# Optimization experiments

Measured on AMD Instinct MI355X. Metric: run time of the kernel, lower is better.

Reference implementation:

```python
import jax, jax.numpy as jnp
import numpy as np
from itertools import product


def _build_apot_levels(num_bits=8, n=2):
    k = num_bits // n
    groups = []
    for i in range(n):
        vals = [0.0]
        for j in range(2 ** k - 1):
            vals.append(2 ** (-(i + j * n)))
        groups.append(vals)
    levels = set()
    for combo in product(*groups):
        levels.add(round(sum(combo), 14))
    levels = sorted(levels)
    max_v = max(levels) if levels else 1.0
    if max_v > 0:
        levels = [v / max_v for v in levels]
    return levels


def _make_levels(num_bits=8, signed=True):
    levels = _build_apot_levels(num_bits=num_bits, n=2)
    if signed:
        neg = [-v for v in levels[1:]][::-1]
        levels = neg + levels
    return np.asarray(levels, dtype=np.float32)


def setup_inputs() -> dict:
    key = jax.random.key(0)
    x = jax.random.normal(key, (32, 4096, 1024), dtype=jnp.float32)
    alpha = jnp.ones((1,), dtype=jnp.float32)          # learned scalar scale
    levels = jnp.asarray(_make_levels(8, True))         # sorted APoT levels buffer, shape [L]
    return {"x": x, "alpha": alpha, "levels": levels}


def reference(x, alpha, levels):
    a = jnp.abs(alpha) + 1e-8                 # [1], broadcasts
    x_norm = jnp.clip(x / a, -1.0, 1.0)       # signed=True clamp
    x_det = jax.lax.stop_gradient(x_norm)
    L = levels.shape[0]
    # torch.bucketize(right=False) == searchsorted side='left'
    idx_right = jnp.clip(jnp.searchsorted(levels, x_det, side="left"), 0, L - 1)
    idx_left = jnp.clip(idx_right - 1, 0, L - 1)
    right = levels[idx_right]
    left = levels[idx_left]
    choose_right = jnp.abs(x_det - left) > jnp.abs(right - x_det)
    snapped = jnp.where(choose_right, right, left)
    # straight-through estimator
    snapped_ste = x_norm + jax.lax.stop_gradient(snapped - x_norm)
    return a * snapped_ste
```

## Files before the change

kernel.cpp:

```cpp
#include <hip/hip_runtime.h>
#include <float.h>


#define TREE_H 9
#define NNODES (1 << TREE_H)

typedef float floatx4 __attribute__((ext_vector_type(4)));

__device__ __forceinline__ float apot_one(float xi, float a,
                                          const float* __restrict__ eyt,
                                          float lev0, float levmax) {
    float xn = xi / a;
    xn = fminf(fmaxf(xn, -1.0f), 1.0f);
    int idx = 1;
    float lft = lev0;
    float rgt = levmax;
    #pragma unroll
    for (int s = 0; s < TREE_H; ++s) {
        float e = eyt[idx];
        bool go_r = e < xn;
        lft = go_r ? e : lft;
        rgt = go_r ? rgt : e;
        idx = 2 * idx + (go_r ? 1 : 0);
    }
    float d_l = fabsf(xn - lft);
    float d_r = fabsf(rgt - xn);
    return a * ((d_l > d_r) ? rgt : lft);
}

__global__ __launch_bounds__(256) void apot_kernel(
    const float* __restrict__ x,
    const float* __restrict__ alpha,
    const float* __restrict__ levels,
    float* __restrict__ out,
    long long n, long long n4, int L)
{
    __shared__ float eyt[NNODES];
    for (int i = threadIdx.x + 1; i < NNODES; i += blockDim.x) {
        int d = 31 - __clz(i);
        int pos = i - (1 << d);
        int srt = pos * (1 << (TREE_H - d)) + (1 << (TREE_H - 1 - d)) - 1;
        eyt[i] = (srt < L) ? levels[srt] : FLT_MAX;
    }
    __syncthreads();

    float a = fabsf(alpha[0]) + 1e-8f;
    float lev0 = levels[0];
    float levmax = levels[L - 1];

    long long tid = (long long)blockIdx.x * blockDim.x + threadIdx.x;
    long long stride = (long long)gridDim.x * blockDim.x;

    const floatx4* __restrict__ x4 = (const floatx4*)x;
    floatx4* __restrict__ o4 = (floatx4*)out;
    for (long long t = tid; t < n4; t += stride) {
        floatx4 v = x4[t];
        floatx4 ov;
        ov.x = apot_one(v.x, a, eyt, lev0, levmax);
        ov.y = apot_one(v.y, a, eyt, lev0, levmax);
        ov.z = apot_one(v.z, a, eyt, lev0, levmax);
        ov.w = apot_one(v.w, a, eyt, lev0, levmax);
        __builtin_nontemporal_store(ov, &o4[t]);
    }
    for (long long t = n4 * 4 + tid; t < n; t += stride) {
        out[t] = apot_one(x[t], a, eyt, lev0, levmax);
    }
}

extern "C" void kernel_launch(void* const* d_in, const int* in_sizes, int n_in,
                              void* d_out, int out_size, void* d_ws, size_t ws_size,
                              hipStream_t stream) {
    const float* x      = (const float*)d_in[0];
    const float* alpha  = (const float*)d_in[1];
    const float* levels = (const float*)d_in[2];
    float* out = (float*)d_out;

    long long n  = (long long)out_size;
    long long n4 = n >> 2;
    int L = in_sizes[2];

    const int block = 256;
    long long want = (n4 + block - 1) / block;
    if (want < 1) want = 1;
    int grid = (int)(want < 8192 ? want : 8192);

    apot_kernel<<<grid, block, 0, stream>>>(x, alpha, levels, out, n, n4, L);
}
```

Measured before the change: 886.0 us.

## Fold symmetric APoT levels into magnitude search with register-held top tree levels

For L==511 the kernel relies on the level table being symmetric around zero. It searches only the positive half using |x|, with a one-ulp bias so ties on negative inputs resolve the same way as the reference, which shortens the Eytzinger search from 9 to 8 levels. The top three tree levels are kept in registers, leaving only 5 shared-memory lookups per element. A specialised path skips the divide and multiply when alpha==1. This assumes symmetric levels, which the general 511-level input may not satisfy, and it adds code size and register pressure.

```diff
diff --git a/kernel.cpp b/kernel.cpp
--- a/kernel.cpp
+++ b/kernel.cpp
@@ -2,10 +2,106 @@
 #include <float.h>
 
 
+typedef float floatx4 __attribute__((ext_vector_type(4)));
+
+
+template<bool AONE>
+__device__ __forceinline__ float apot_fold(
+    float xi, float a, const float* __restrict__ eyt, float zl,
+    float e1, float e2, float e3, float e4, float e5, float e6, float e7)
+{
+    float xn = AONE ? xi : (xi / a);
+    xn = fminf(fmaxf(xn, -1.0f), 1.0f);
+    bool neg = xn < 0.0f;
+    float u  = fabsf(xn);
+    float us = __uint_as_float(__float_as_uint(u) + (neg ? 1u : 0u));
+
+    float lft = zl;
+    float rgt = FLT_MAX;
+
+    bool g0 = e1 < us;  lft = g0 ? e1 : lft;  rgt = g0 ? rgt : e1;
+    float ea = g0 ? e3 : e2;
+    bool g1 = ea < us;  lft = g1 ? ea : lft;  rgt = g1 ? rgt : ea;
+    float t0 = g1 ? e5 : e4;
+    float t1 = g1 ? e7 : e6;
+    float eb = g0 ? t1 : t0;
+    bool g2 = eb < us;  lft = g2 ? eb : lft;  rgt = g2 ? rgt : eb;
+
+    int idx = 8 + (g0 ? 4 : 0) + (g1 ? 2 : 0) + (g2 ? 1 : 0);
+    #pragma unroll
+    for (int s = 0; s < 5; ++s) {
+        float e = eyt[idx];
+        bool g = e < us;
+        lft = g ? e : lft;
+        rgt = g ? rgt : e;
+        idx = 2 * idx + (g ? 1 : 0);
+    }
+
+    float dl = u - lft;
+    float dr = rgt - u;
+    bool cr = neg ? (dl >= dr) : (dl > dr);
+    float mag = cr ? rgt : lft;
+    float res = AONE ? mag : (a * mag);
+    res = neg ? -res : res;
+    return res + 0.0f;
+}
+
+template<bool AONE>
+__device__ __forceinline__ void apot_loop_511(
+    const float* __restrict__ x, float* __restrict__ out,
+    long long n, long long n4, float a, float zl,
+    const float* __restrict__ eyt,
+    float e1, float e2, float e3, float e4, float e5, float e6, float e7)
+{
+    long long tid = (long long)blockIdx.x * blockDim.x + threadIdx.x;
+    long long stride = (long long)gridDim.x * blockDim.x;
+    const floatx4* __restrict__ x4 = (const floatx4*)x;
+    floatx4* __restrict__ o4 = (floatx4*)out;
+    for (long long t = tid; t < n4; t += stride) {
+        floatx4 v = x4[t];
+        floatx4 ov;
+        ov.x = apot_fold<AONE>(v.x, a, eyt, zl, e1, e2, e3, e4, e5, e6, e7);
+        ov.y = apot_fold<AONE>(v.y, a, eyt, zl, e1, e2, e3, e4, e5, e6, e7);
+        ov.z = apot_fold<AONE>(v.z, a, eyt, zl, e1, e2, e3, e4, e5, e6, e7);
+        ov.w = apot_fold<AONE>(v.w, a, eyt, zl, e1, e2, e3, e4, e5, e6, e7);
+        __builtin_nontemporal_store(ov, &o4[t]);
+    }
+    for (long long t = n4 * 4 + tid; t < n; t += stride) {
+        out[t] = apot_fold<AONE>(x[t], a, eyt, zl, e1, e2, e3, e4, e5, e6, e7);
+    }
+}
+
+__global__ __launch_bounds__(256) void apot_kernel_511(
+    const float* __restrict__ x,
+    const float* __restrict__ alpha,
+    const float* __restrict__ levels,
+    float* __restrict__ out,
+    long long n, long long n4)
+{
+    __shared__ float eyt[256];
+    for (int i = threadIdx.x + 1; i < 256; i += blockDim.x) {
+        int d = 31 - __clz(i);
+        int pos = i - (1 << d);
+        int srt = pos * (1 << (8 - d)) + (1 << (7 - d)) - 1;
+        eyt[i] = levels[256 + srt];
+    }
+    __syncthreads();
+
+    float a  = fabsf(alpha[0]) + 1e-8f;
+    float zl = levels[255];
+    float e1 = eyt[1], e2 = eyt[2], e3 = eyt[3], e4 = eyt[4],
+          e5 = eyt[5], e6 = eyt[6], e7 = eyt[7];
+
+    if (a == 1.0f) {
+        apot_loop_511<true >(x, out, n, n4, a, zl, eyt, e1, e2, e3, e4, e5, e6, e7);
+    } else {
+        apot_loop_511<false>(x, out, n, n4, a, zl, eyt, e1, e2, e3, e4, e5, e6, e7);
+    }
+}
+
+
 #define TREE_H 9
 #define NNODES (1 << TREE_H)
-
-typedef float floatx4 __attribute__((ext_vector_type(4)));
 
 __device__ __forceinline__ float apot_one(float xi, float a,
                                           const float* __restrict__ eyt,
@@ -84,5 +180,9 @@
     if (want < 1) want = 1;
     int grid = (int)(want < 8192 ? want : 8192);
 
-    apot_kernel<<<grid, block, 0, stream>>>(x, alpha, levels, out, n, n4, L);
+    if (L == 511) {
+        apot_kernel_511<<<grid, block, 0, stream>>>(x, alpha, levels, out, n, n4);
+    } else {
+        apot_kernel<<<grid, block, 0, stream>>>(x, alpha, levels, out, n, n4, L);
+    }
 }
```

Result: no change. 879.2 us (-0.8%).
